# Performance work log

Measured on AMD Instinct MI355X. Metric: run time of the kernel, lower is better.

Reference implementation:

```python
import jax, jax.numpy as jnp
import numpy as np

N_HEADS = 16
DIM = 1024
DH = DIM // N_HEADS  # 64
B, S = 4, 2048


def setup_inputs() -> dict:
    key = jax.random.key(0)
    k1, k2, k3, k4 = jax.random.split(key, 4)
    x = jax.random.normal(k1, (B, S, DIM), dtype=jnp.float32)
    src_mask = jax.random.uniform(k2, (B, S)) < 0.1
    # torch nn.Linear weights: y = x @ W.T
    W_qkv = jax.random.normal(k3, (3 * DIM, DIM), dtype=jnp.float32) * (DIM ** -0.5)
    W_o = jax.random.normal(k4, (DIM, DIM), dtype=jnp.float32) * (DIM ** -0.5)
    return {"x": x, "src_mask": src_mask, "W_qkv": W_qkv, "W_o": W_o}


def reference(x, src_mask, W_qkv, W_o):
    b, s, _ = x.shape
    qkv = x @ W_qkv.T  # [b, s, 3*DIM]
    # rearrange 'b s (n_h d) -> ... ' BEFORE chunk(3): head h owns a contiguous
    # 3*DH slice, which is then split into q,k,v of DH each.
    qkv = qkv.reshape(b, s, N_HEADS, 3 * DH)
    q, k, v = jnp.split(qkv, 3, axis=-1)  # each [b, s, h, dh]
    logits = jnp.einsum('bqhd,bkhd->bhqk', q, k) * (DH ** -0.5)
    logits = jnp.where(src_mask[:, None, None, :], -jnp.inf, logits)
    attn = jax.nn.softmax(logits, axis=-1)  # dropout=0.0 -> identity
    out = jnp.einsum('bhqk,bkhd->bqhd', attn, v).reshape(b, s, DIM)
    return out @ W_o.T
```

## Files before the change

kernel.cpp:

```cpp
#include <hip/hip_runtime.h>
#include <hip/hip_bf16.h>
#include <stdint.h>


typedef unsigned short u16;
typedef __attribute__((ext_vector_type(8))) short     bf16x8;
typedef __attribute__((ext_vector_type(8))) unsigned short u16x8;
typedef __attribute__((ext_vector_type(4))) unsigned short u16x4;
typedef __attribute__((ext_vector_type(4))) float     f32x4;
typedef __attribute__((ext_vector_type(4))) int       i32x4;

#define DEVI __device__ __forceinline__

DEVI u16 f2bf(float f) {
    union { float f; uint32_t u; } v; v.f = f;
    uint32_t r = v.u + 0x7fffu + ((v.u >> 16) & 1u);
    return (u16)(r >> 16);
}

DEVI u16 f2bf_cvt(float f) {
    __hip_bfloat16 h = __float2bfloat16(f);
    return __builtin_bit_cast(u16, h);
}

#define GLDS(gp, lp) __builtin_amdgcn_global_load_lds( \
    (const __attribute__((address_space(1))) void*)(gp), \
    (__attribute__((address_space(3))) void*)(lp), 16, 0, 0)

#define MFMA16(a, b, c) __builtin_amdgcn_mfma_f32_16x16x32_bf16(a, b, c, 0, 0, 0)

#define QSCALE 0.1803368801111204f

__global__ __launch_bounds__(256) void cvt_f32_bf16(const float* __restrict__ in,
                                                    u16* __restrict__ out, int n4) {
    int i = blockIdx.x * 256 + threadIdx.x;
    if (i >= n4) return;
    f32x4 v = *(const f32x4*)(in + (size_t)i * 4);
    u16x4 o;
#pragma unroll
    for (int j = 0; j < 4; j++) o[j] = f2bf(v[j]);
    *(u16x4*)(out + (size_t)i * 4) = o;
}

template <int MODE>
__global__ __launch_bounds__(256) void gemm_bt(const u16* __restrict__ A,
                                               const u16* __restrict__ B,
                                               void* __restrict__ C,
                                               int M, int N, int K) {
    __shared__ u16 As[128 * 32];
    __shared__ u16 Bs[128 * 32];
    const int lane = threadIdx.x & 63;
    const int wave = threadIdx.x >> 6;
    const int mT = blockIdx.y * 128;
    const int nT = blockIdx.x * 128;

    const int srow = wave * 16 + (lane >> 2);
    const int skc  = (lane & 3) * 8;
    const u16* gA = A + (size_t)(mT + srow) * K + skc;
    const u16* gB = B + (size_t)(nT + srow) * K + skc;
    u16* lA = As + wave * 512;
    u16* lB = Bs + wave * 512;

    f32x4 acc[4][4];
#pragma unroll
    for (int m = 0; m < 4; m++)
#pragma unroll
        for (int n = 0; n < 4; n++) acc[m][n] = f32x4{0.f, 0.f, 0.f, 0.f};

    const int wm = (wave >> 1) * 64, wn = (wave & 1) * 64;
    const int fr = lane & 15, fg = lane >> 4;

    for (int kt = 0; kt < K; kt += 32) {
        GLDS(gA + kt, lA);
        GLDS(gA + kt + (size_t)64 * K, lA + 2048);
        GLDS(gB + kt, lB);
        GLDS(gB + kt + (size_t)64 * K, lB + 2048);
        __syncthreads();
        bf16x8 af[4], bg[4];
#pragma unroll
        for (int m = 0; m < 4; m++)
            af[m] = *(const bf16x8*)(As + (wm + m * 16 + fr) * 32 + fg * 8);
#pragma unroll
        for (int n = 0; n < 4; n++)
            bg[n] = *(const bf16x8*)(Bs + (wn + n * 16 + fr) * 32 + fg * 8);
#pragma unroll
        for (int m = 0; m < 4; m++)
#pragma unroll
            for (int n = 0; n < 4; n++)
                acc[m][n] = MFMA16(af[m], bg[n], acc[m][n]);
        __syncthreads();
    }

    float qs[4];
#pragma unroll
    for (int n = 0; n < 4; n++) {
        if (MODE == 2) {
            int col = nT + wn + n * 16 + fr;
            qs[n] = ((col % 192) < 64) ? QSCALE : 1.0f;
        } else qs[n] = 1.0f;
    }
#pragma unroll
    for (int m = 0; m < 4; m++)
#pragma unroll
        for (int r = 0; r < 4; r++) {
            int row = mT + wm + m * 16 + fg * 4 + r;
#pragma unroll
            for (int n = 0; n < 4; n++) {
                int col = nT + wn + n * 16 + fr;
                if (MODE == 0) ((float*)C)[(size_t)row * N + col] = acc[m][n][r];
                else           ((u16*)C)[(size_t)row * N + col] = f2bf(acc[m][n][r] * qs[n]);
            }
        }
}

__global__ __launch_bounds__(256) void transpose_v(const u16* __restrict__ qkv,
                                                   u16* __restrict__ vT) {
    __shared__ u16 tile[64][72];
    const int tid = threadIdx.x;
    const int b = blockIdx.z, h = blockIdx.y;
    const int s0 = blockIdx.x * 64;
    const int r = tid >> 3, c = tid & 7;

#pragma unroll
    for (int p = 0; p < 2; p++) {
        int s = p * 32 + r;
        u16x8 v = *(const u16x8*)(qkv + (size_t)(b * 2048 + s0 + s) * 3072
                                  + h * 192 + 128 + c * 8);
#pragma unroll
        for (int j = 0; j < 8; j++) tile[c * 8 + j][s] = v[j];
    }
    __syncthreads();
#pragma unroll
    for (int p = 0; p < 2; p++) {
        int d = p * 32 + r;
        u16x8 v = *(const u16x8*)(&tile[d][c * 8]);
        *(u16x8*)(vT + ((size_t)((b * 16 + h) * 64 + d)) * 2048 + s0 + c * 8) = v;
    }
}

__global__ __launch_bounds__(512) void attn_kernel(const u16* __restrict__ qkv,
                                                   const u16* __restrict__ vT,
                                                   const int* __restrict__ mask,
                                                   u16* __restrict__ ctx) {
    __shared__ u16 Kl[2][4096];
    __shared__ u16 Vl[2][4096];
    __shared__ u16 Pl[8][16 * 80];
    __shared__ float madd[2048];

    const int lane = threadIdx.x & 63;
    const int wave = threadIdx.x >> 6;

    const int fid = blockIdx.x + 16 * blockIdx.y + 256 * blockIdx.z;
    const int swz = (fid & 7) * 128 + (fid >> 3);
    const int b = swz >> 8, h = (swz >> 4) & 15;
    const int qT = (swz & 15) * 128;
    const int fr = lane & 15, fg = lane >> 4;

    {
        const i32x4* mp = (const i32x4*)(mask + b * 2048);
        i32x4 m0 = mp[threadIdx.x];
        f32x4 a0;
#pragma unroll
        for (int j = 0; j < 4; j++) a0[j] = m0[j] ? -3e30f : 0.0f;
        ((f32x4*)madd)[threadIdx.x] = a0;
    }

    const u16* qbase = qkv + (size_t)(b * 2048 + qT + wave * 16 + fr) * 3072 + h * 192;
    const bf16x8 aq0 = *(const bf16x8*)(qbase + fg * 8);
    const bf16x8 aq1 = *(const bf16x8*)(qbase + 32 + fg * 8);

    const int srow = wave * 8 + (lane >> 3);
    const int sch  = (lane & 7) ^ (srow & 7);
    const u16* kg = qkv + (size_t)(b * 2048 + srow) * 3072 + h * 192 + 64 + sch * 8;
    const u16* vg = vT + ((size_t)((b * 16 + h) * 64) + srow) * 2048 + sch * 8;

    {
        GLDS(kg, Kl[0] + wave * 512);
        GLDS(vg, Vl[0] + wave * 512);
    }

    f32x4 so[4];
#pragma unroll
    for (int n = 0; n < 4; n++) so[n] = f32x4{0.f, 0.f, 0.f, 0.f};
    f32x4 lacc = f32x4{0.f, 0.f, 0.f, 0.f};
    u16* pw = Pl[wave];

    const short onebf = (short)0x3F80;
    const bf16x8 vones = {onebf, onebf, onebf, onebf, onebf, onebf, onebf, onebf};

    __syncthreads();

    int buf = 0;
    for (int t = 0; t < 32; ++t) {
        if (t < 31) {
            GLDS(kg + (size_t)(t + 1) * (64 * 3072), Kl[buf ^ 1] + wave * 512);
            GLDS(vg + (size_t)(t + 1) * 64,          Vl[buf ^ 1] + wave * 512);
        }
        const u16* kc = Kl[buf];
        const int kb = t * 64;

        f32x4 s[4];
#pragma unroll
        for (int n = 0; n < 4; n++) s[n] = *(const f32x4*)&madd[kb + n * 16 + fg * 4];
#pragma unroll
        for (int n = 0; n < 4; n++) {
            const u16* krp = kc + (n * 16 + fr) * 64;
            bf16x8 ka0 = *(const bf16x8*)(krp + ((fg ^ (fr & 7)) * 8));
            bf16x8 ka1 = *(const bf16x8*)(krp + (((4 + fg) ^ (fr & 7)) * 8));
            s[n] = MFMA16(ka0, aq0, s[n]);
            s[n] = MFMA16(ka1, aq1, s[n]);
        }

#pragma unroll
        for (int n = 0; n < 4; n++)
#pragma unroll
            for (int r = 0; r < 4; r++) s[n][r] = exp2f(s[n][r]);

#pragma unroll
        for (int n = 0; n < 4; n++) {
            u16x4 pk;
#pragma unroll
            for (int r = 0; r < 4; r++) pk[r] = f2bf_cvt(s[n][r]);
            *(u16x4*)(pw + fr * 80 + n * 16 + fg * 4) = pk;
        }
        asm volatile("s_waitcnt lgkmcnt(0)" ::: "memory");

        const u16* vc = Vl[buf];
#pragma unroll
        for (int ks = 0; ks < 2; ks++) {
            bf16x8 pa = *(const bf16x8*)(pw + fr * 80 + ks * 32 + fg * 8);
#pragma unroll
            for (int n = 0; n < 4; n++) {
                bf16x8 bv = *(const bf16x8*)(vc + (n * 16 + fr) * 64
                                             + (((ks * 4 + fg) ^ (fr & 7)) * 8));
                so[n] = MFMA16(pa, bv, so[n]);
            }
            lacc = MFMA16(pa, vones, lacc);
        }

        __syncthreads();
        buf ^= 1;
    }

#pragma unroll
    for (int r = 0; r < 4; r++) {
        const int q = qT + wave * 16 + fg * 4 + r;
        const float inv = 1.0f / lacc[r];
#pragma unroll
        for (int n = 0; n < 4; n++)
            ctx[(size_t)(b * 2048 + q) * 1024 + h * 64 + n * 16 + fr] = f2bf(so[n][r] * inv);
    }
}

extern "C" void kernel_launch(void* const* d_in, const int* in_sizes, int n_in,
                              void* d_out, int out_size, void* d_ws, size_t ws_size,
                              hipStream_t stream) {
    const float* x    = (const float*)d_in[0];
    const int*   mask = (const int*)d_in[1];
    const float* Wqkv = (const float*)d_in[2];
    const float* Wo   = (const float*)d_in[3];
    float* out = (float*)d_out;

    char* ws = (char*)d_ws;
    u16* xb    = (u16*)(ws);
    u16* wqkvb = (u16*)(ws + 16777216);
    u16* wob   = (u16*)(ws + 23068672);
    u16* qkvb  = (u16*)(ws + 25165824);
    u16* ctxb  = (u16*)(ws + 75497472);
    u16* vTb   = xb;

    cvt_f32_bf16<<<8192, 256, 0, stream>>>(x, xb, 8388608 / 4);
    cvt_f32_bf16<<<3072, 256, 0, stream>>>(Wqkv, wqkvb, 3145728 / 4);
    cvt_f32_bf16<<<1024, 256, 0, stream>>>(Wo, wob, 1048576 / 4);

    gemm_bt<2><<<dim3(24, 64), 256, 0, stream>>>(xb, wqkvb, qkvb, 8192, 3072, 1024);
    transpose_v<<<dim3(32, 16, 4), 256, 0, stream>>>(qkvb, vTb);
    attn_kernel<<<dim3(16, 16, 4), 512, 0, stream>>>(qkvb, vTb, mask, ctxb);
    gemm_bt<0><<<dim3(8, 64), 256, 0, stream>>>(ctxb, wob, out, 8192, 1024, 1024);
}
```

Measured before the change: 243.4 us.

## Rewrite attention with 32x32 MFMA, register-resident P via permlane swap, mask folded into V

```diff
diff --git a/kernel.cpp b/kernel.cpp
--- a/kernel.cpp
+++ b/kernel.cpp
@@ -4,11 +4,13 @@
 
 
 typedef unsigned short u16;
-typedef __attribute__((ext_vector_type(8))) short     bf16x8;
-typedef __attribute__((ext_vector_type(8))) unsigned short u16x8;
-typedef __attribute__((ext_vector_type(4))) unsigned short u16x4;
-typedef __attribute__((ext_vector_type(4))) float     f32x4;
-typedef __attribute__((ext_vector_type(4))) int       i32x4;
+typedef __attribute__((ext_vector_type(8)))  short    bf16x8;
+typedef __attribute__((ext_vector_type(8)))  unsigned short u16x8;
+typedef __attribute__((ext_vector_type(4)))  unsigned short u16x4;
+typedef __attribute__((ext_vector_type(4)))  float    f32x4;
+typedef __attribute__((ext_vector_type(16))) float    f32x16;
+typedef __attribute__((ext_vector_type(4)))  unsigned int u32x4;
+typedef __attribute__((ext_vector_type(4)))  int      i32x4;
 
 #define DEVI __device__ __forceinline__
 
@@ -18,16 +20,15 @@
     return (u16)(r >> 16);
 }
 
-DEVI u16 f2bf_cvt(float f) {
-    __hip_bfloat16 h = __float2bfloat16(f);
-    return __builtin_bit_cast(u16, h);
-}
-
 #define GLDS(gp, lp) __builtin_amdgcn_global_load_lds( \
     (const __attribute__((address_space(1))) void*)(gp), \
     (__attribute__((address_space(3))) void*)(lp), 16, 0, 0)
 
 #define MFMA16(a, b, c) __builtin_amdgcn_mfma_f32_16x16x32_bf16(a, b, c, 0, 0, 0)
+#define MFMA32(a, b, c) __builtin_amdgcn_mfma_f32_32x32x16_bf16(a, b, c, 0, 0, 0)
+
+#define CVTPK(d, lo, hi) asm("v_cvt_pk_bf16_f32 %0, %1, %2" : "=v"(d) : "v"(lo), "v"(hi))
+#define PLSWAP(a, b) asm("v_permlane32_swap_b32 %0, %1" : "+v"(a), "+v"(b))
 
 #define QSCALE 0.1803368801111204f
 
@@ -114,6 +115,7 @@
 }
 
 __global__ __launch_bounds__(256) void transpose_v(const u16* __restrict__ qkv,
+                                                   const int* __restrict__ mask,
                                                    u16* __restrict__ vT) {
     __shared__ u16 tile[64][72];
     const int tid = threadIdx.x;
@@ -126,6 +128,7 @@
         int s = p * 32 + r;
         u16x8 v = *(const u16x8*)(qkv + (size_t)(b * 2048 + s0 + s) * 3072
                                   + h * 192 + 128 + c * 8);
+        if (mask[b * 2048 + s0 + s]) v = u16x8{0, 0, 0, 0, 0, 0, 0, 0};
 #pragma unroll
         for (int j = 0; j < 8; j++) tile[c * 8 + j][s] = v[j];
     }
@@ -138,104 +141,114 @@
     }
 }
 
-__global__ __launch_bounds__(512) void attn_kernel(const u16* __restrict__ qkv,
-                                                   const u16* __restrict__ vT,
-                                                   const int* __restrict__ mask,
-                                                   u16* __restrict__ ctx) {
+__global__ __launch_bounds__(256, 3) void attn_kernel(const u16* __restrict__ qkv,
+                                                      const u16* __restrict__ vT,
+                                                      const int* __restrict__ mask,
+                                                      u16* __restrict__ ctx) {
     __shared__ u16 Kl[2][4096];
     __shared__ u16 Vl[2][4096];
-    __shared__ u16 Pl[8][16 * 80];
-    __shared__ float madd[2048];
+    __shared__ u16 keeps[2048];
 
     const int lane = threadIdx.x & 63;
     const int wave = threadIdx.x >> 6;
+    const int hl = lane >> 5;
+    const int l31 = lane & 31;
 
     const int fid = blockIdx.x + 16 * blockIdx.y + 256 * blockIdx.z;
     const int swz = (fid & 7) * 128 + (fid >> 3);
     const int b = swz >> 8, h = (swz >> 4) & 15;
     const int qT = (swz & 15) * 128;
-    const int fr = lane & 15, fg = lane >> 4;
 
     {
-        const i32x4* mp = (const i32x4*)(mask + b * 2048);
-        i32x4 m0 = mp[threadIdx.x];
-        f32x4 a0;
-#pragma unroll
-        for (int j = 0; j < 4; j++) a0[j] = m0[j] ? -3e30f : 0.0f;
-        ((f32x4*)madd)[threadIdx.x] = a0;
-    }
-
-    const u16* qbase = qkv + (size_t)(b * 2048 + qT + wave * 16 + fr) * 3072 + h * 192;
-    const bf16x8 aq0 = *(const bf16x8*)(qbase + fg * 8);
-    const bf16x8 aq1 = *(const bf16x8*)(qbase + 32 + fg * 8);
-
-    const int srow = wave * 8 + (lane >> 3);
-    const int sch  = (lane & 7) ^ (srow & 7);
-    const u16* kg = qkv + (size_t)(b * 2048 + srow) * 3072 + h * 192 + 64 + sch * 8;
-    const u16* vg = vT + ((size_t)((b * 16 + h) * 64) + srow) * 2048 + sch * 8;
-
-    {
-        GLDS(kg, Kl[0] + wave * 512);
-        GLDS(vg, Vl[0] + wave * 512);
-    }
-
-    f32x4 so[4];
-#pragma unroll
-    for (int n = 0; n < 4; n++) so[n] = f32x4{0.f, 0.f, 0.f, 0.f};
-    f32x4 lacc = f32x4{0.f, 0.f, 0.f, 0.f};
-    u16* pw = Pl[wave];
-
-    const short onebf = (short)0x3F80;
-    const bf16x8 vones = {onebf, onebf, onebf, onebf, onebf, onebf, onebf, onebf};
+        const i32x4* mp = (const i32x4*)(mask + b * 2048) + threadIdx.x * 2;
+        i32x4 m0 = mp[0], m1 = mp[1];
+        u16x8 kp;
+#pragma unroll
+        for (int j = 0; j < 4; j++) {
+            kp[j]     = m0[j] ? (u16)0 : (u16)0x3F80;
+            kp[4 + j] = m1[j] ? (u16)0 : (u16)0x3F80;
+        }
+        *(u16x8*)(keeps + threadIdx.x * 8) = kp;
+    }
+
+    const u16* qrow = qkv + (size_t)(b * 2048 + qT + wave * 32 + l31) * 3072 + h * 192;
+    bf16x8 aq[4];
+#pragma unroll
+    for (int c = 0; c < 4; c++) aq[c] = *(const bf16x8*)(qrow + c * 16 + hl * 8);
+
+    const int r0 = wave * 16 + (lane >> 3);
+    const int j0 = (lane & 7) ^ (r0 & 7);
+    const u16* kg = qkv + (size_t)(b * 2048 + r0) * 3072 + h * 192 + 64 + j0 * 8;
+    const u16* vg = vT + ((size_t)((b * 16 + h) * 64) + r0) * 2048 + j0 * 8;
+
+#define STAGE(tt, bb) do { \
+        const u16* kgp = kg + (size_t)(tt) * (64 * 3072); \
+        const u16* vgp = vg + (size_t)(tt) * 64; \
+        u16* lK = Kl[bb] + wave * 1024; \
+        u16* lV = Vl[bb] + wave * 1024; \
+        GLDS(kgp, lK); GLDS(kgp + (size_t)8 * 3072, lK + 512); \
+        GLDS(vgp, lV); GLDS(vgp + (size_t)8 * 2048, lV + 512); \
+    } while (0)
+
+    STAGE(0, 0);
+
+    f32x16 so0, so1, lacc;
+#pragma unroll
+    for (int i = 0; i < 16; i++) { so0[i] = 0.f; so1[i] = 0.f; lacc[i] = 0.f; }
+
+    const int swc = l31 & 7;
 
     __syncthreads();
 
     int buf = 0;
     for (int t = 0; t < 32; ++t) {
-        if (t < 31) {
-            GLDS(kg + (size_t)(t + 1) * (64 * 3072), Kl[buf ^ 1] + wave * 512);
-            GLDS(vg + (size_t)(t + 1) * 64,          Vl[buf ^ 1] + wave * 512);
-        }
+        if (t < 31) STAGE(t + 1, buf ^ 1);
         const u16* kc = Kl[buf];
+        const u16* vc = Vl[buf];
         const int kb = t * 64;
 
-        f32x4 s[4];
-#pragma unroll
-        for (int n = 0; n < 4; n++) s[n] = *(const f32x4*)&madd[kb + n * 16 + fg * 4];
-#pragma unroll
-        for (int n = 0; n < 4; n++) {
-            const u16* krp = kc + (n * 16 + fr) * 64;
-            bf16x8 ka0 = *(const bf16x8*)(krp + ((fg ^ (fr & 7)) * 8));
-            bf16x8 ka1 = *(const bf16x8*)(krp + (((4 + fg) ^ (fr & 7)) * 8));
-            s[n] = MFMA16(ka0, aq0, s[n]);
-            s[n] = MFMA16(ka1, aq1, s[n]);
-        }
-
-#pragma unroll
-        for (int n = 0; n < 4; n++)
-#pragma unroll
-            for (int r = 0; r < 4; r++) s[n][r] = exp2f(s[n][r]);
-
-#pragma unroll
-        for (int n = 0; n < 4; n++) {
-            u16x4 pk;
-#pragma unroll
-            for (int r = 0; r < 4; r++) pk[r] = f2bf_cvt(s[n][r]);
-            *(u16x4*)(pw + fr * 80 + n * 16 + fg * 4) = pk;
-        }
-        asm volatile("s_waitcnt lgkmcnt(0)" ::: "memory");
-
-        const u16* vc = Vl[buf];
-#pragma unroll
-        for (int ks = 0; ks < 2; ks++) {
-            bf16x8 pa = *(const bf16x8*)(pw + fr * 80 + ks * 32 + fg * 8);
-#pragma unroll
-            for (int n = 0; n < 4; n++) {
-                bf16x8 bv = *(const bf16x8*)(vc + (n * 16 + fr) * 64
-                                             + (((ks * 4 + fg) ^ (fr & 7)) * 8));
-                so[n] = MFMA16(pa, bv, so[n]);
-            }
-            lacc = MFMA16(pa, vones, lacc);
+        f32x16 s0, s1;
+#pragma unroll
+        for (int i = 0; i < 16; i++) { s0[i] = 0.f; s1[i] = 0.f; }
+#pragma unroll
+        for (int c = 0; c < 4; c++) {
+            const int ch = ((c * 2 + hl) ^ swc) * 8;
+            bf16x8 ka0 = *(const bf16x8*)(kc + l31 * 64 + ch);
+            bf16x8 ka1 = *(const bf16x8*)(kc + (32 + l31) * 64 + ch);
+            s0 = MFMA32(ka0, aq[c], s0);
+            s1 = MFMA32(ka1, aq[c], s1);
+        }
+
+#pragma unroll
+        for (int i = 0; i < 16; i++) { s0[i] = exp2f(s0[i]); s1[i] = exp2f(s1[i]); }
+
+        uint32_t u0, u1, u2, u3, u4, u5, u6, u7;
+        bf16x8 pa0, pa1, pa2, pa3;
+        CVTPK(u0, s0[0], s0[1]);  CVTPK(u1, s0[2], s0[3]);
+        CVTPK(u2, s0[4], s0[5]);  CVTPK(u3, s0[6], s0[7]);
+        CVTPK(u4, s0[8], s0[9]);  CVTPK(u5, s0[10], s0[11]);
+        CVTPK(u6, s0[12], s0[13]); CVTPK(u7, s0[14], s0[15]);
+        PLSWAP(u0, u2); PLSWAP(u1, u3); PLSWAP(u4, u6); PLSWAP(u5, u7);
+        pa0 = __builtin_bit_cast(bf16x8, u32x4{u0, u1, u2, u3});
+        pa1 = __builtin_bit_cast(bf16x8, u32x4{u4, u5, u6, u7});
+        CVTPK(u0, s1[0], s1[1]);  CVTPK(u1, s1[2], s1[3]);
+        CVTPK(u2, s1[4], s1[5]);  CVTPK(u3, s1[6], s1[7]);
+        CVTPK(u4, s1[8], s1[9]);  CVTPK(u5, s1[10], s1[11]);
+        CVTPK(u6, s1[12], s1[13]); CVTPK(u7, s1[14], s1[15]);
+        PLSWAP(u0, u2); PLSWAP(u1, u3); PLSWAP(u4, u6); PLSWAP(u5, u7);
+        pa2 = __builtin_bit_cast(bf16x8, u32x4{u0, u1, u2, u3});
+        pa3 = __builtin_bit_cast(bf16x8, u32x4{u4, u5, u6, u7});
+
+#pragma unroll
+        for (int c = 0; c < 4; c++) {
+            const bf16x8 pa = (c == 0) ? pa0 : (c == 1) ? pa1 : (c == 2) ? pa2 : pa3;
+            const int ch = ((c * 2 + hl) ^ swc) * 8;
+            bf16x8 bv0 = *(const bf16x8*)(vc + l31 * 64 + ch);
+            bf16x8 bv1 = *(const bf16x8*)(vc + (32 + l31) * 64 + ch);
+            bf16x8 kp  = *(const bf16x8*)(keeps + kb + c * 16 + hl * 8);
+            so0 = MFMA32(pa, bv0, so0);
+            so1 = MFMA32(pa, bv1, so1);
+            lacc = MFMA32(pa, kp, lacc);
         }
 
         __syncthreads();
@@ -243,13 +256,14 @@
     }
 
 #pragma unroll
-    for (int r = 0; r < 4; r++) {
-        const int q = qT + wave * 16 + fg * 4 + r;
+    for (int r = 0; r < 16; r++) {
+        const int q = qT + wave * 32 + (r & 3) + 8 * (r >> 2) + 4 * hl;
         const float inv = 1.0f / lacc[r];
-#pragma unroll
-        for (int n = 0; n < 4; n++)
-            ctx[(size_t)(b * 2048 + q) * 1024 + h * 64 + n * 16 + fr] = f2bf(so[n][r] * inv);
-    }
+        u16* crow = ctx + (size_t)(b * 2048 + q) * 1024 + h * 64 + l31;
+        crow[0]  = f2bf(so0[r] * inv);
+        crow[32] = f2bf(so1[r] * inv);
+    }
+#undef STAGE
 }
 
 extern "C" void kernel_launch(void* const* d_in, const int* in_sizes, int n_in,
@@ -274,7 +288,7 @@
     cvt_f32_bf16<<<1024, 256, 0, stream>>>(Wo, wob, 1048576 / 4);
 
     gemm_bt<2><<<dim3(24, 64), 256, 0, stream>>>(xb, wqkvb, qkvb, 8192, 3072, 1024);
-    transpose_v<<<dim3(32, 16, 4), 256, 0, stream>>>(qkvb, vTb);
-    attn_kernel<<<dim3(16, 16, 4), 512, 0, stream>>>(qkvb, vTb, mask, ctxb);
+    transpose_v<<<dim3(32, 16, 4), 256, 0, stream>>>(qkvb, mask, vTb);
+    attn_kernel<<<dim3(16, 16, 4), 256, 0, stream>>>(qkvb, vTb, mask, ctxb);
     gemm_bt<0><<<dim3(8, 64), 256, 0, stream>>>(ctxb, wob, out, 8192, 1024, 1024);
 }
```

New measurement: 233.8 us. -3.9%, faster.
